# Kernel optimization log

Hardware: AMD Instinct MI355X
Metric: run time of the kernel (lower is better)

Reference implementation:

```python
import jax, jax.numpy as jnp
import numpy as np

N_NODES = 4096
N_EDGES = 100000
N_PAIRS = 1000000
MAX_PATH = 5
EDGE_DIM = 16


def setup_inputs() -> dict:
    key = jax.random.key(0)
    k1, k2, k3, k4, k5, k6 = jax.random.split(key, 6)
    x = jax.random.normal(k1, (N_NODES, EDGE_DIM), dtype=jnp.float32)
    edge_attr = jax.random.normal(k2, (N_EDGES, EDGE_DIM), dtype=jnp.float32)
    edge_vector = jax.random.normal(k3, (MAX_PATH, EDGE_DIM), dtype=jnp.float32)
    # unique (src, dst) pairs so the scatter-set is well-defined (matches the
    # dict-of-dicts edge_paths, where each (src, dst) appears at most once)
    pair_ids = jax.random.permutation(k4, N_NODES * N_NODES)[:N_PAIRS]
    src_idx = (pair_ids // N_NODES).astype(jnp.int64)
    dst_idx = (pair_ids % N_NODES).astype(jnp.int64)
    # ragged paths: random length in [1, MAX_PATH], padded with -1
    path_idx = jax.random.randint(k5, (N_PAIRS, MAX_PATH), 0, N_EDGES).astype(jnp.int64)
    lengths = jax.random.randint(k6, (N_PAIRS, 1), 1, MAX_PATH + 1)
    valid = jnp.arange(MAX_PATH)[None, :] < lengths
    path_idx = jnp.where(valid, path_idx, -1)
    return {"x": x, "edge_attr": edge_attr, "edge_vector": edge_vector,
            "src_idx": src_idx, "dst_idx": dst_idx, "path_idx": path_idx}


def reference(x, edge_attr, edge_vector, src_idx, dst_idx, path_idx):
    # path_idx: [P, L] edge indices, -1 = padding beyond the path length
    n = x.shape[0]
    mask = path_idx >= 0                                   # [P, L]
    safe = jnp.where(mask, path_idx, 0)
    feats = edge_attr[safe]                                # [P, L, D] irregular gather
    dots = jnp.einsum('pld,ld->pl', feats, edge_vector)    # per-hop dot products
    dots = jnp.where(mask, dots, 0.0)
    cnt = mask.sum(axis=-1)                                # path lengths
    # mean over the path; empty path -> 0 (matches nan_to_num on 0/0)
    vals = jnp.where(cnt > 0, dots.sum(axis=-1) / jnp.maximum(cnt, 1).astype(dots.dtype), 0.0)
    cij = jnp.zeros((n, n), dtype=x.dtype).at[src_idx, dst_idx].set(vals)
    return cij
```

## Files before the change

### kernel.cpp

```cpp
#include <hip/hip_runtime.h>

#define N_NODES  4096
#define MAX_PATH 5
#define EDGE_DIM 16

__global__ __launch_bounds__(256) void precompute_dots_kernel(
    const float* __restrict__ edge_attr,
    const float* __restrict__ edge_vector,
    float*       __restrict__ D,
    int n_edges)
{
    int e = blockIdx.x * blockDim.x + threadIdx.x;
    if (e >= n_edges) return;

    const float4* ea = (const float4*)(edge_attr + (size_t)e * EDGE_DIM);
    float4 a0 = ea[0], a1 = ea[1], a2 = ea[2], a3 = ea[3];

#pragma unroll
    for (int l = 0; l < MAX_PATH; ++l) {
        const float4* ev = (const float4*)(edge_vector + l * EDGE_DIM);
        float4 b0 = ev[0], b1 = ev[1], b2 = ev[2], b3 = ev[3];
        float d = a0.x*b0.x + a0.y*b0.y + a0.z*b0.z + a0.w*b0.w
                + a1.x*b1.x + a1.y*b1.y + a1.z*b1.z + a1.w*b1.w
                + a2.x*b2.x + a2.y*b2.y + a2.z*b2.z + a2.w*b2.w
                + a3.x*b3.x + a3.y*b3.y + a3.z*b3.z + a3.w*b3.w;
        D[(size_t)l * n_edges + e] = d;
    }
}

__global__ __launch_bounds__(256) void edge_encoding_kernel(
    const float* __restrict__ D,
    const int*   __restrict__ src_idx,
    const int*   __restrict__ dst_idx,
    const int*   __restrict__ path_idx,
    float*       __restrict__ out,
    int n_pairs, int n_edges)
{
    int p = blockIdx.x * blockDim.x + threadIdx.x;
    if (p >= n_pairs) return;

    int e[MAX_PATH];
#pragma unroll
    for (int l = 0; l < MAX_PATH; ++l)
        e[l] = path_idx[(size_t)p * MAX_PATH + l];

    float sum = 0.0f;
    int   cnt = 0;
#pragma unroll
    for (int l = 0; l < MAX_PATH; ++l) {
        if (e[l] >= 0) {
            sum += D[(size_t)l * n_edges + e[l]];
            ++cnt;
        }
    }

    float val = (cnt > 0) ? (sum / (float)cnt) : 0.0f;
    out[(size_t)src_idx[p] * N_NODES + dst_idx[p]] = val;
}

extern "C" void kernel_launch(void* const* d_in, const int* in_sizes, int n_in,
                              void* d_out, int out_size, void* d_ws, size_t ws_size,
                              hipStream_t stream)
{
    const float* edge_attr   = (const float*)d_in[1];
    const float* edge_vector = (const float*)d_in[2];
    const int*   src_idx     = (const int*)d_in[3];
    const int*   dst_idx     = (const int*)d_in[4];
    const int*   path_idx    = (const int*)d_in[5];
    float*       out         = (float*)d_out;
    float*       D           = (float*)d_ws;

    const int n_edges = in_sizes[1] / EDGE_DIM;
    const int n_pairs = in_sizes[3];

    hipMemsetAsync(d_out, 0, (size_t)out_size * sizeof(float), stream);

    const int block = 256;
    precompute_dots_kernel<<<(n_edges + block - 1) / block, block, 0, stream>>>(
        edge_attr, edge_vector, D, n_edges);

    edge_encoding_kernel<<<(n_pairs + block - 1) / block, block, 0, stream>>>(
        D, src_idx, dst_idx, path_idx, out, n_pairs, n_edges);
}
```

Before: 47.87 us.

## Split pair processing into vectorized gather and scatter kernels

Splits the fused per-pair kernel into a gather kernel that computes path means for two pairs per thread with 8-byte vector loads of path indices, and a scatter kernel that writes four values per thread using vector loads of vals/src/dst. This is meant to improve load coalescing and separate the irregular D gathers from the random 64MB-output scatter. In exchange it adds an extra launch and a round trip of the 4MB vals buffer through global memory, and the gather kernel assumes n_pairs is even.

```diff
diff --git a/kernel.cpp b/kernel.cpp
--- a/kernel.cpp
+++ b/kernel.cpp
@@ -3,6 +3,9 @@
 #define N_NODES  4096
 #define MAX_PATH 5
 #define EDGE_DIM 16
+
+typedef int   iv2 __attribute__((ext_vector_type(2)));
+typedef float fv2 __attribute__((ext_vector_type(2)));
 
 __global__ __launch_bounds__(256) void precompute_dots_kernel(
     const float* __restrict__ edge_attr,
@@ -28,34 +31,68 @@
     }
 }
 
-__global__ __launch_bounds__(256) void edge_encoding_kernel(
+__global__ __launch_bounds__(256) void gather_vals_kernel(
     const float* __restrict__ D,
-    const int*   __restrict__ src_idx,
-    const int*   __restrict__ dst_idx,
     const int*   __restrict__ path_idx,
-    float*       __restrict__ out,
+    float*       __restrict__ vals,
     int n_pairs, int n_edges)
 {
-    int p = blockIdx.x * blockDim.x + threadIdx.x;
-    if (p >= n_pairs) return;
+    int t  = blockIdx.x * blockDim.x + threadIdx.x;
+    int p0 = t * 2;
+    if (p0 >= n_pairs) return;
 
-    int e[MAX_PATH];
+    const iv2* pp = (const iv2*)(path_idx + (size_t)p0 * MAX_PATH);
+    iv2 w0 = pp[0], w1 = pp[1], w2 = pp[2], w3 = pp[3], w4 = pp[4];
+    int e[10] = { w0.x, w0.y, w1.x, w1.y, w2.x,
+                  w2.y, w3.x, w3.y, w4.x, w4.y };
+
+    float g[10];
 #pragma unroll
-    for (int l = 0; l < MAX_PATH; ++l)
-        e[l] = path_idx[(size_t)p * MAX_PATH + l];
-
-    float sum = 0.0f;
-    int   cnt = 0;
+    for (int j = 0; j < 2; ++j) {
 #pragma unroll
-    for (int l = 0; l < MAX_PATH; ++l) {
-        if (e[l] >= 0) {
-            sum += D[(size_t)l * n_edges + e[l]];
-            ++cnt;
+        for (int l = 0; l < MAX_PATH; ++l) {
+            int idx = e[j * MAX_PATH + l];
+            g[j * MAX_PATH + l] = (idx >= 0) ? D[(size_t)l * n_edges + idx] : 0.0f;
         }
     }
 
-    float val = (cnt > 0) ? (sum / (float)cnt) : 0.0f;
-    out[(size_t)src_idx[p] * N_NODES + dst_idx[p]] = val;
+    fv2 v;
+#pragma unroll
+    for (int j = 0; j < 2; ++j) {
+        float sum = 0.0f;
+        int   cnt = 0;
+#pragma unroll
+        for (int l = 0; l < MAX_PATH; ++l) {
+            if (e[j * MAX_PATH + l] >= 0) { sum += g[j * MAX_PATH + l]; ++cnt; }
+        }
+        v[j] = (cnt > 0) ? (sum / (float)cnt) : 0.0f;
+    }
+    *(fv2*)(vals + p0) = v;
+}
+
+__global__ __launch_bounds__(256) void scatter_vals_kernel(
+    const float* __restrict__ vals,
+    const int*   __restrict__ src_idx,
+    const int*   __restrict__ dst_idx,
+    float*       __restrict__ out,
+    int n_pairs)
+{
+    int t  = blockIdx.x * blockDim.x + threadIdx.x;
+    int p0 = t * 4;
+    if (p0 >= n_pairs) return;
+
+    if (p0 + 3 < n_pairs) {
+        float4 v  = *(const float4*)(vals + p0);
+        int4   sv = *(const int4*)(src_idx + p0);
+        int4   dv = *(const int4*)(dst_idx + p0);
+        out[(size_t)sv.x * N_NODES + dv.x] = v.x;
+        out[(size_t)sv.y * N_NODES + dv.y] = v.y;
+        out[(size_t)sv.z * N_NODES + dv.z] = v.z;
+        out[(size_t)sv.w * N_NODES + dv.w] = v.w;
+    } else {
+        for (int p = p0; p < n_pairs; ++p)
+            out[(size_t)src_idx[p] * N_NODES + dst_idx[p]] = vals[p];
+    }
 }
 
 extern "C" void kernel_launch(void* const* d_in, const int* in_sizes, int n_in,
@@ -68,10 +105,12 @@
     const int*   dst_idx     = (const int*)d_in[4];
     const int*   path_idx    = (const int*)d_in[5];
     float*       out         = (float*)d_out;
-    float*       D           = (float*)d_ws;
 
     const int n_edges = in_sizes[1] / EDGE_DIM;
     const int n_pairs = in_sizes[3];
+
+    float* D    = (float*)d_ws;
+    float* vals = (float*)((char*)d_ws + ((size_t)5 * n_edges * sizeof(float) + 1023 & ~(size_t)1023));
 
     hipMemsetAsync(d_out, 0, (size_t)out_size * sizeof(float), stream);
 
@@ -79,6 +118,11 @@
     precompute_dots_kernel<<<(n_edges + block - 1) / block, block, 0, stream>>>(
         edge_attr, edge_vector, D, n_edges);
 
-    edge_encoding_kernel<<<(n_pairs + block - 1) / block, block, 0, stream>>>(
-        D, src_idx, dst_idx, path_idx, out, n_pairs, n_edges);
+    const int tA = (n_pairs + 1) / 2;
+    gather_vals_kernel<<<(tA + block - 1) / block, block, 0, stream>>>(
+        D, path_idx, vals, n_pairs, n_edges);
+
+    const int tB = (n_pairs + 3) / 4;
+    scatter_vals_kernel<<<(tB + block - 1) / block, block, 0, stream>>>(
+        vals, src_idx, dst_idx, out, n_pairs);
 }
```

Result: slower. 51.75 us (+8.1%).
